# Performance work log

Hardware: AMD Instinct MI355X
Metric: run time of the kernel (lower is better)

The kernel has to match this reference:

```python
import jax, jax.numpy as jnp
from jax import lax
import numpy as np

HD = 256  # hidden_dim

def _conv(x, w, b=None, pad=1, groups=1):
    y = lax.conv_general_dilated(x, w, (1, 1), [(pad, pad), (pad, pad)],
                                 feature_group_count=groups,
                                 dimension_numbers=('NCHW', 'OIHW', 'NCHW'))
    return y if b is None else y + b[None, :, None, None]

def _maxpool2(x):
    return lax.reduce_window(x, -jnp.inf, lax.max, (1, 1, 2, 2), (1, 1, 2, 2), 'VALID')

def _up2(x):
    return jnp.repeat(jnp.repeat(x, 2, axis=2), 2, axis=3)

def setup_inputs() -> dict:
    key = jax.random.key(0)
    ks = jax.random.split(key, 17)
    w = lambda k, s: jax.random.normal(k, s, jnp.float32) * 0.05
    return {
        'x': jax.random.normal(ks[0], (8, 16, 3, 84, 84), jnp.float32),
        'enc_w1': w(ks[1], (64, 3, 3, 3)),    'enc_b1': w(ks[2], (64,)),
        'enc_w2': w(ks[3], (128, 64, 3, 3)),  'enc_b2': w(ks[4], (128,)),
        'enc_w3': w(ks[5], (256, 128, 3, 3)), 'enc_b3': w(ks[6], (256,)),
        'dw_w': w(ks[7], (512, 1, 3, 3)),
        'pw_w': w(ks[8], (1024, 512, 1, 1)),  'pw_b': w(ks[9], (1024,)),
        'dec_w1': w(ks[10], (128, 256, 3, 3)), 'dec_b1': w(ks[11], (128,)),
        'dec_w2': w(ks[12], (64, 128, 3, 3)),  'dec_b2': w(ks[13], (64,)),
        'dec_w3': w(ks[14], (1, 64, 1, 1)),    'dec_b3': w(ks[15], (1,)),
    }

def reference(x, enc_w1, enc_b1, enc_w2, enc_b2, enc_w3, enc_b3,
              dw_w, pw_w, pw_b, dec_w1, dec_b1, dec_w2, dec_b2, dec_w3, dec_b3):
    B, T, C, H, W = x.shape
    xf = x.reshape(B * T, C, H, W)
    # encoder: conv-relu-pool, conv-relu-pool, conv-relu
    f = _maxpool2(jax.nn.relu(_conv(xf, enc_w1, enc_b1)))
    f = _maxpool2(jax.nn.relu(_conv(f, enc_w2, enc_b2)))
    f = jax.nn.relu(_conv(f, enc_w3, enc_b3))           # [B*T, 256, 21, 21]
    Hf, Wf = f.shape[2], f.shape[3]
    feats = f.reshape(B, T, HD, Hf, Wf).transpose(1, 0, 2, 3, 4)  # [T,B,256,Hf,Wf]

    h0 = jnp.zeros((B, HD, Hf, Wf), x.dtype)
    c0 = jnp.zeros((B, HD, Hf, Wf), x.dtype)

    def step(carry, ft):
        h, c = carry
        comb = jnp.concatenate([ft, h], axis=1)          # [B, 512, Hf, Wf]
        g = _conv(comb, dw_w, None, pad=1, groups=comb.shape[1])  # depthwise
        g = _conv(g, pw_w, pw_b, pad=0)                  # pointwise -> 4*HD gates
        i, fg, o, gg = jnp.split(g, 4, axis=1)
        c2 = jax.nn.sigmoid(fg) * c + jax.nn.sigmoid(i) * jnp.tanh(gg)
        h2 = jax.nn.sigmoid(o) * jnp.tanh(c2)
        return (h2, c2), h2

    (h, c), hs = lax.scan(step, (h0, c0), feats)
    hs = hs.transpose(1, 0, 2, 3, 4).reshape(B * T, HD, Hf, Wf)

    # decoder: up2-conv-relu, up2-conv-relu, conv1x1
    d = jax.nn.relu(_conv(_up2(hs), dec_w1, dec_b1))     # [B*T, 128, 42, 42]
    d = jax.nn.relu(_conv(_up2(d), dec_w2, dec_b2))      # [B*T, 64, 84, 84]
    out = _conv(d, dec_w3, dec_b3, pad=0)                # [B*T, 1, 84, 84]
    out = out.reshape(B, T, 1, 84, 84)
    return out, h, c
```

## Files before the change

### kernel.cpp

```cpp
#include <hip/hip_runtime.h>
#include <hip/hip_bf16.h>

typedef __hip_bfloat16 bf16;
typedef __attribute__((ext_vector_type(8))) short bf16x8;
typedef __attribute__((ext_vector_type(4))) float f32x4;
#define DEV static __device__ __forceinline__

DEV float b2f(bf16 v) { return __bfloat162float(v); }
DEV bf16  f2b(float v) { return __float2bfloat16(v); }
DEV unsigned short f2u(float v) { bf16 t = f2b(v); return *(unsigned short*)&t; }
DEV float u2f(unsigned short u) { bf16 t = *(bf16*)&u; return __bfloat162float(t); }
DEV float sigf(float x) { return 1.0f / (1.0f + __expf(-x)); }
DEV float tanhfast(float x) { return 2.0f / (1.0f + __expf(-2.0f * x)) - 1.0f; }


__global__ void k_detect(const unsigned short* __restrict__ xb, int nscan, int* flag)
{
    __shared__ int cnt_s[256];
    int tid = threadIdx.x;
    int c = 0;
    for (int i = tid; i < nscan; i += 256) {
        unsigned int e = (xb[i] >> 7) & 0xFF;
        c += (e >= 0xC0);
    }
// ... 7 lines not shown
}

struct CanonSrc { const void* s[15]; };

__global__ __launch_bounds__(256) void k_canon_all(
    CanonSrc cs, char* __restrict__ wsb, int total, const int* __restrict__ flag)
{
    static const __device__ int off_d[16] = {0, 1728, 1792, 75520, 75648, 370560,
        370816, 375424, 899712, 900736, 1195648, 1195776, 1269504, 1269568,
        1269632, 1269633};
    static const __device__ long woff_d[15] = {0, 3456, 3584, 151040, 151296,
        741120, 741632, 750848, 1799424, 1801472, 2391296, 2391552, 2539008,
        2539136, 2539264};
    int i = blockIdx.x * 256 + threadIdx.x;
    if (i >= total) return;
    int t = 0;
    while (t < 14 && i >= off_d[t + 1]) ++t;
    int j = i - off_d[t];
    bf16* dst = (bf16*)(wsb + woff_d[t]);
    if (*flag) dst[j] = f2b(((const float*)cs.s[t])[j]);
    else       dst[j] = ((const bf16*)cs.s[t])[j];
}

__global__ __launch_bounds__(256) void k_combine1(
    const bf16* __restrict__ w, bf16* __restrict__ wc1)
{
    int idx = blockIdx.x * 256 + threadIdx.x;
    if (idx >= 524288) return;
    int ci = idx & 255, tap = (idx >> 8) & 3;
    int oc = (idx >> 10) & 127, par = idx >> 17;
    int a = tap >> 1, b = tap & 1;
    int py = par >> 1, px = par & 1;
    const bf16* wb = w + (oc * 256 + ci) * 9;
    float v = 0.f;
    #pragma unroll
    for (int ky = 0; ky < 3; ++ky) {
        bool rok = (py == 0) ? (a == 0 ? (ky == 0) : (ky >= 1))
                             : (a == 0 ? (ky <= 1) : (ky == 2));
        if (!rok) continue;
        #pragma unroll
        for (int kx = 0; kx < 3; ++kx) {
            bool cok = (px == 0) ? (b == 0 ? (kx == 0) : (kx >= 1))
                                 : (b == 0 ? (kx <= 1) : (kx == 2));
            if (cok) v += b2f(wb[ky * 3 + kx]);
        }
    }
    wc1[idx] = f2b(v);
}

__global__ __launch_bounds__(256) void k_combine2(
    const bf16* __restrict__ w, bf16* __restrict__ wc2)
{
    int idx = blockIdx.x * 256 + threadIdx.x;
    if (idx >= 131072) return;
    int ci = idx & 127, tap = (idx >> 7) & 3;
    int oc = (idx >> 9) & 63, par = idx >> 15;
    int a = tap >> 1, b = tap & 1;
    int py = par >> 1, px = par & 1;
    const bf16* wb = w + (oc * 128 + ci) * 9;
    float v = 0.f;
    #pragma unroll
    for (int ky = 0; ky < 3; ++ky) {
        bool rok = (py == 0) ? (a == 0 ? (ky == 0) : (ky >= 1))
                             : (a == 0 ? (ky <= 1) : (ky == 2));
        if (!rok) continue;
        #pragma unroll
        for (int kx = 0; kx < 3; ++kx) {
            bool cok = (px == 0) ? (b == 0 ? (kx == 0) : (kx >= 1))
                                 : (b == 0 ? (kx <= 1) : (kx == 2));
            if (cok) v += b2f(wb[ky * 3 + kx]);
        }
    }
    wc2[idx] = f2b(v);
}

__global__ __launch_bounds__(256) void k_prep_pw(
    const bf16* __restrict__ pww, bf16* __restrict__ wcp)
{
    int idx = blockIdx.x * 256 + threadIdx.x;
    if (idx >= 524288) return;
    int k = idx & 511, m = idx >> 9;
    int ch = m >> 2, gate = m & 3;
    wcp[idx] = pww[(gate * 256 + ch) * 512 + k];
}

__global__ __launch_bounds__(256) void k_prep_w3(
    const bf16* __restrict__ w, bf16* __restrict__ wc3)
{
    int idx = blockIdx.x * 256 + threadIdx.x;
    if (idx >= 294912) return;
    int oc = idx / 1152, rem = idx % 1152;
    int tap = rem >> 7, ci = rem & 127;
    wc3[idx] = w[(oc * 128 + ci) * 9 + tap];
}

__global__ __launch_bounds__(256) void k_prep_w2(
    const bf16* __restrict__ w, bf16* __restrict__ wc2e)
{
    int idx = blockIdx.x * 256 + threadIdx.x;
    if (idx >= 73728) return;
    int oc = idx / 576, rem = idx % 576;
    int tap = rem >> 6, ci = rem & 63;
    wc2e[idx] = w[(oc * 64 + ci) * 9 + tap];
}

__global__ __launch_bounds__(256) void k_prep_w1(
    const bf16* __restrict__ w, bf16* __restrict__ wc1e)
{
    int idx = blockIdx.x * 256 + threadIdx.x;
    if (idx >= 2048) return;
    int oc = idx >> 5, k = idx & 31;
    bf16 v = f2b(0.f);
    if (k < 27) v = w[oc * 27 + k];
    wc1e[idx] = v;
}

__global__ __launch_bounds__(256) void k_prep_dwt(
    const bf16* __restrict__ w, bf16* __restrict__ dwt)
{
    int idx = blockIdx.x * 256 + threadIdx.x;
    if (idx >= 4608) return;
    int tap = idx >> 9, ch = idx & 511;
    dwt[idx] = w[ch * 9 + tap];
}

__global__ __launch_bounds__(256) void k_conv1_mfma(
    const void* __restrict__ xv, const bf16* __restrict__ wc1e,
    const bf16* __restrict__ bias, bf16* __restrict__ p1c, int fbase,
    const int* __restrict__ flag)
{
    __shared__ __align__(16) short W_s[64 * 40];
    __shared__ __align__(16) short H_s[3 * 6 * 88];
    const int nt = blockIdx.x, z = blockIdx.z;
    const int n = fbase + z;
    const int tid = threadIdx.x;
    const int wave = tid >> 6, lane = tid & 63;
    const int quad = lane >> 4, nl = lane & 15;
    const int nn = wave * 16 + nl;
    const int p0 = nt * 63, y0 = p0 / 42;
    const int np = p0 + ((nn < 63) ? nn : 62);
    const int y = np / 42, xq = np % 42;
    const int isf32 = *flag;
    for (int u = tid; u < 256; u += 256) {
        int m = u >> 2, k8 = (u & 3) * 8;
        *(uint4*)&W_s[m * 40 + k8] = *(const uint4*)&wc1e[m * 32 + k8];
    }
// ... 40 lines not shown
    }
    if (nn < 63) {
        #pragma unroll
        for (int f = 0; f < 4; ++f) {
            ushort4 o;
            unsigned short* op = (unsigned short*)&o;
            #pragma unroll
            for (int reg = 0; reg < 4; ++reg) {
                const int oc = f * 16 + quad * 4 + reg;
                float m = fmaxf(fmaxf(acc[0][f][reg], acc[1][f][reg]),
                                fmaxf(acc[2][f][reg], acc[3][f][reg]));
                op[reg] = f2u(fmaxf(m + b2f(bias[oc]), 0.f));
            }
            *(ushort4*)&p1c[((long)z * 1764 + np) * 64 + f * 16 + quad * 4] = o;
        }
    }
}

__global__ __launch_bounds__(256) void k_conv2_mfma(
    const bf16* __restrict__ p1c, const bf16* __restrict__ wc2e,
    const bf16* __restrict__ bias, bf16* __restrict__ p2c)
{
    __shared__ __align__(16) short H_s[352 * 72];
    __shared__ __align__(16) short W_s[128 * 40];
    const int nt = blockIdx.x, z = blockIdx.z;
    const int tid = threadIdx.x;
    const int wave = tid >> 6, lane = tid & 63;
    const int quad = lane >> 4, nl = lane & 15;
    const int nn = wave * 16 + nl;
    const int np = (nn < 63) ? nn : 62;
    const int iyl = np / 21, ix = np % 21;
    const int r0 = nt * 3;
    for (int u = tid; u < 2816; u += 256) {
        int rc = u >> 3, c8 = u & 7;
        int gy = 2 * r0 - 1 + rc / 44, gx = (rc % 44) - 1;
        uint4 v = {0, 0, 0, 0};
        if (gy >= 0 && gy < 42 && gx >= 0 && gx < 42)
            v = *(const uint4*)&p1c[((long)z * 1764 + gy * 42 + gx) * 64 + c8 * 8];
        *(uint4*)&H_s[rc * 72 + c8 * 8] = v;
    }
    f32x4 acc[4][8];
    #pragma unroll
    for (int p = 0; p < 4; ++p)
        #pragma unroll
        for (int f = 0; f < 8; ++f) acc[p][f] = (f32x4){0.f, 0.f, 0.f, 0.f};
    for (int tap = 0; tap < 9; ++tap) {
        const int dy = tap / 3, dx = tap % 3;
        for (int cc = 0; cc < 2; ++cc) {
            __syncthreads();
            for (int u = tid; u < 512; u += 256) {
                int m = u >> 2, k8 = (u & 3) * 8;
                *(uint4*)&W_s[m * 40 + k8] =
                    *(const uint4*)&wc2e[m * 576 + tap * 64 + cc * 32 + k8];
            }
            __syncthreads();
            bf16x8 af[8];
            #pragma unroll
            for (int f = 0; f < 8; ++f)
                af[f] = *(const bf16x8*)&W_s[(f * 16 + nl) * 40 + quad * 8];
            #pragma unroll
            for (int par = 0; par < 4; ++par) {
                const int pa = par >> 1, pb = par & 1;
                const int hy = 2 * iyl + pa + dy;
                const int hx = 2 * ix + pb + dx;
                const bf16x8 bv =
                    *(const bf16x8*)&H_s[(hy * 44 + hx) * 72 + cc * 32 + quad * 8];
                #pragma unroll
                for (int f = 0; f < 8; ++f)
                    acc[par][f] = __builtin_amdgcn_mfma_f32_16x16x32_bf16(
                        af[f], bv, acc[par][f], 0, 0, 0);
            }
        }
    }
    if (nn < 63) {
        #pragma unroll
        for (int f = 0; f < 8; ++f) {
            ushort4 o;
            unsigned short* op = (unsigned short*)&o;
            #pragma unroll
            for (int reg = 0; reg < 4; ++reg) {
                const int oc = f * 16 + quad * 4 + reg;
                float m = fmaxf(fmaxf(acc[0][f][reg], acc[1][f][reg]),
                                fmaxf(acc[2][f][reg], acc[3][f][reg]));
                op[reg] = f2u(fmaxf(m + b2f(bias[oc]), 0.f));
            }
            *(ushort4*)&p2c[((long)z * 441 + (r0 + iyl) * 21 + ix) * 128 +
                            f * 16 + quad * 4] = o;
        }
    }
}

__global__ __launch_bounds__(256) void k_conv3_mfma(
    const bf16* __restrict__ p2c, const bf16* __restrict__ wc3,
    const bf16* __restrict__ bias, bf16* __restrict__ feats, int fbase)
{
    __shared__ __align__(16) short H_s[115 * 136];
    __shared__ __align__(16) short W_s[128 * 40];
    const int nt = blockIdx.x, oq = blockIdx.y, z = blockIdx.z;
    const int n = fbase + z;
    const int slot = (n & 15) * 8 + (n >> 4);
    const int tid = threadIdx.x;
    const int wave = tid >> 6, lane = tid & 63;
    const int quad = lane >> 4, nl = lane & 15;
    const int nn = wave * 16 + nl;
    const int np = (nn < 63) ? nn : 62;
    const int iyl = np / 21, ox = np % 21;
    const int r0 = nt * 3;
    for (int u = tid; u < 1840; u += 256) {
        int rc = u >> 4, c8 = u & 15;
        int gy = r0 + rc / 23 - 1, gx = (rc % 23) - 1;
        uint4 v = {0, 0, 0, 0};
        if (gy >= 0 && gy < 21 && gx >= 0 && gx < 21)
            v = *(const uint4*)&p2c[((long)z * 441 + gy * 21 + gx) * 128 + c8 * 8];
        *(uint4*)&H_s[rc * 136 + c8 * 8] = v;
    }
    f32x4 acc[8];
    #pragma unroll
    for (int f = 0; f < 8; ++f) acc[f] = (f32x4){0.f, 0.f, 0.f, 0.f};
    const int hb = iyl * 23 + ox;
    for (int tap = 0; tap < 9; ++tap) {
        const int dy = tap / 3, dx = tap % 3;
        const int hofs = (hb + dy * 23 + dx) * 136;
        for (int cc = 0; cc < 4; ++cc) {
            __syncthreads();
            for (int u = tid; u < 512; u += 256) {
                int m = u >> 2, k8 = (u & 3) * 8;
                *(uint4*)&W_s[m * 40 + k8] =
                    *(const uint4*)&wc3[(oq * 128 + m) * 1152 + tap * 128 + cc * 32 + k8];
            }
            __syncthreads();
            const bf16x8 bv = *(const bf16x8*)&H_s[hofs + cc * 32 + quad * 8];
            #pragma unroll
            for (int f = 0; f < 8; ++f) {
                bf16x8 af = *(const bf16x8*)&W_s[(f * 16 + nl) * 40 + quad * 8];
                acc[f] = __builtin_amdgcn_mfma_f32_16x16x32_bf16(af, bv, acc[f], 0, 0, 0);
            }
        }
    }
    if (nn < 63) {
        const int oy = r0 + iyl;
        #pragma unroll
        for (int f = 0; f < 8; ++f) {
            ushort4 o;
            unsigned short* op = (unsigned short*)&o;
            #pragma unroll
            for (int reg = 0; reg < 4; ++reg) {
                const int oc = oq * 128 + f * 16 + quad * 4 + reg;
                op[reg] = f2u(fmaxf(acc[f][reg] + b2f(bias[oc]), 0.f));
            }
            *(ushort4*)&feats[((long)slot * 441 + oy * 21 + ox) * 256 +
                              oq * 128 + f * 16 + quad * 4] = o;
        }
    }
}

__global__ __launch_bounds__(256) void k_dw_vec(
    const bf16* __restrict__ feats, const float* __restrict__ h,
    const bf16* __restrict__ dwt, bf16* __restrict__ dwout, int t)
{
    int idx = blockIdx.x * 256 + threadIdx.x;
// ... 29 lines not shown
                const float4 x1 = *(const float4*)&hb_[(ny * 21 + nx) * 256 + ch - 252];
                const float xf[8] = {x0.x, x0.y, x0.z, x0.w, x1.x, x1.y, x1.z, x1.w};
                #pragma unroll
                for (int j = 0; j < 8; ++j)
                    a8[j] += u2f(((unsigned short*)&wv)[j]) * xf[j];
            }
        }
    }
    ushort4 o0, o1;
    #pragma unroll
    for (int j = 0; j < 4; ++j) {
        ((unsigned short*)&o0)[j] = f2u(a8[j]);
        ((unsigned short*)&o1)[j] = f2u(a8[4 + j]);
    }
    *(ushort4*)&dwout[((long)b * 441 + p) * 512 + ch] = o0;
    *(ushort4*)&dwout[((long)b * 441 + p) * 512 + ch + 4] = o1;
}

__global__ __launch_bounds__(256) void k_pw_mfma(
    const bf16* __restrict__ dwout, const bf16* __restrict__ wcp,
    const bf16* __restrict__ pwb, float* __restrict__ h, float* __restrict__ c,
    bf16* __restrict__ hst)
{
    __shared__ __align__(16) short W_s[128 * 72];
    __shared__ __align__(16) short X_s[64 * 72];
    __shared__ bf16 pb_s[1024];
    const int nt = blockIdx.x, mq = blockIdx.y, b = blockIdx.z;
    const int tid = threadIdx.x;
    const int wave = tid >> 6, lane = tid & 63;
    const int quad = lane >> 4, nl = lane & 15;
    const int nn = wave * 16 + nl;
    for (int i = tid; i < 1024; i += 256) pb_s[i] = pwb[i];
    f32x4 acc[8];
    #pragma unroll
    for (int f = 0; f < 8; ++f) acc[f] = (f32x4){0.f, 0.f, 0.f, 0.f};
    for (int cc = 0; cc < 8; ++cc) {
        __syncthreads();
        for (int u = tid; u < 1024; u += 256) {
            int m = u >> 3, k8 = (u & 7) * 8;
            *(uint4*)&W_s[m * 72 + k8] =
                *(const uint4*)&wcp[(mq * 128 + m) * 512 + cc * 64 + k8];
        }
        for (int u = tid; u < 512; u += 256) {
            int p = u >> 3, k8 = (u & 7) * 8;
            int gp = nt * 63 + p;
            uint4 v = {0, 0, 0, 0};
            if (p < 63)
                v = *(const uint4*)&dwout[((long)b * 441 + gp) * 512 + cc * 64 + k8];
            *(uint4*)&X_s[p * 72 + k8] = v;
        }
        __syncthreads();
        #pragma unroll
        for (int s = 0; s < 2; ++s) {
            const bf16x8 bv = *(const bf16x8*)&X_s[nn * 72 + s * 32 + quad * 8];
            #pragma unroll
            for (int f = 0; f < 8; ++f) {
                bf16x8 af = *(const bf16x8*)&W_s[(f * 16 + nl) * 72 + s * 32 + quad * 8];
                acc[f] = __builtin_amdgcn_mfma_f32_16x16x32_bf16(af, bv, acc[f], 0, 0, 0);
            }
        }
    }
    if (nn < 63) {
        const int p = nt * 63 + nn;
        #pragma unroll
        for (int f = 0; f < 8; ++f) {
            const int ch = mq * 32 + f * 4 + quad;
            float ig = sigf(acc[f][0] + b2f(pb_s[ch]));
            float fg = sigf(acc[f][1] + b2f(pb_s[256 + ch]));
            float og = sigf(acc[f][2] + b2f(pb_s[512 + ch]));
            float gg = tanhfast(acc[f][3] + b2f(pb_s[768 + ch]));
            const int ci2 = (b * 441 + p) * 256 + ch;
            float c2 = fg * c[ci2] + ig * gg;
            float h2 = og * tanhfast(c2);
            c[ci2] = c2; h[ci2] = h2;
            hst[(long)b * 112896 + p * 256 + ch] = f2b(h2);
        }
    }
}

__global__ __launch_bounds__(256) void k_dec1_mfma(
    const bf16* __restrict__ feats, const bf16* __restrict__ hs0,
    const bf16* __restrict__ wc1, const bf16* __restrict__ bias,
    bf16* __restrict__ d1c, int c0f)
{
    __shared__ __align__(16) short H_s[184 * 72];
    __shared__ __align__(16) short W_s[128 * 72];
    const int nt = blockIdx.x, par = blockIdx.y, z = blockIdx.z;
    const int py = par >> 1, px = par & 1;
    const int n = c0f + z, bb = n >> 4, tt = n & 15;
    const short* hsf = (const short*)((tt == 0) ? (hs0 + (long)bb * 112896)
                        : (feats + (long)((tt - 1) * 8 + bb) * 112896));
    const int tid = threadIdx.x;
    const int wave = tid >> 6, lane = tid & 63;
    const int quad = lane >> 4, nl = lane & 15;
    int maxs = 440 - nt * 126; if (maxs > 125) maxs = 125;
    int hb[2], pv[2]; bool val[2];
    #pragma unroll
    for (int pg = 0; pg < 2; ++pg) {
        int slot = (wave * 2 + pg) * 16 + nl;
        val[pg] = (slot <= maxs);
        int sl = val[pg] ? slot : maxs;
        int p = nt * 126 + sl;
        pv[pg] = p;
        int y = p / 21, x = p % 21;
        hb[pg] = (y - nt * 6 + py) * 23 + (x + px);
    }
    f32x4 acc[2][8];
    #pragma unroll
    for (int pg = 0; pg < 2; ++pg)
        #pragma unroll
        for (int f = 0; f < 8; ++f) acc[pg][f] = (f32x4){0.f, 0.f, 0.f, 0.f};
    for (int cc = 0; cc < 4; ++cc) {
        __syncthreads();
        for (int u = tid; u < 1472; u += 256) {
            int rc = u >> 3, c8 = (u & 7) * 8;
            int gy = nt * 6 - 1 + rc / 23, gx = (rc % 23) - 1;
            uint4 v = {0, 0, 0, 0};
            if (gy >= 0 && gy < 21 && gx >= 0 && gx < 21)
                v = *(const uint4*)&hsf[(gy * 21 + gx) * 256 + cc * 64 + c8];
            *(uint4*)&H_s[rc * 72 + c8] = v;
        }
        for (int tap = 0; tap < 4; ++tap) {
            __syncthreads();
            for (int u = tid; u < 1024; u += 256) {
                int m = u >> 3, k8 = (u & 7) * 8;
                *(uint4*)&W_s[m * 72 + k8] =
                    *(const uint4*)&wc1[((par * 128 + m) << 10) + tap * 256 + cc * 64 + k8];
            }
            __syncthreads();
            const int a = tap >> 1, b = tap & 1;
            #pragma unroll
            for (int s = 0; s < 2; ++s) {
                bf16x8 bv0 = *(const bf16x8*)&H_s[(hb[0] + a * 23 + b) * 72 + s * 32 + quad * 8];
                bf16x8 bv1 = *(const bf16x8*)&H_s[(hb[1] + a * 23 + b) * 72 + s * 32 + quad * 8];
                #pragma unroll
                for (int f = 0; f < 8; ++f) {
                    bf16x8 af = *(const bf16x8*)&W_s[(f * 16 + nl) * 72 + s * 32 + quad * 8];
                    acc[0][f] = __builtin_amdgcn_mfma_f32_16x16x32_bf16(af, bv0, acc[0][f], 0, 0, 0);
                    acc[1][f] = __builtin_amdgcn_mfma_f32_16x16x32_bf16(af, bv1, acc[1][f], 0, 0, 0);
                }
            }
        }
    }
    #pragma unroll
    for (int pg = 0; pg < 2; ++pg) {
        if (!val[pg]) continue;
        const int p = pv[pg];
        const int oy = 2 * (p / 21) + py, ox = 2 * (p % 21) + px;
        #pragma unroll
        for (int f = 0; f < 8; ++f) {
            ushort4 o;
            unsigned short* op = (unsigned short*)&o;
            #pragma unroll
            for (int reg = 0; reg < 4; ++reg) {
                const int oc = f * 16 + quad * 4 + reg;
                op[reg] = f2u(fmaxf(acc[pg][f][reg] + b2f(bias[oc]), 0.f));
            }
            *(ushort4*)&d1c[((long)z * 1764 + oy * 42 + ox) * 128 +
                            f * 16 + quad * 4] = o;
        }
    }
}

__global__ __launch_bounds__(256) void k_dec2f_mfma(
    const bf16* __restrict__ d1c, const bf16* __restrict__ wc2,
    const bf16* __restrict__ bias, const bf16* __restrict__ w3,
    const bf16* __restrict__ b3, void* __restrict__ out, int c0f,
    const int* __restrict__ flag)
{
    __shared__ __align__(16) short H_s[220 * 72];
    __shared__ __align__(16) short W_s[64 * 72];
    const int nt = blockIdx.x, par = blockIdx.y, z = blockIdx.z;
    const int py = par >> 1, px = par & 1;
    const int tid = threadIdx.x;
    const int wave = tid >> 6, lane = tid & 63;
    const int quad = lane >> 4, nl = lane & 15;
    int hb[2], pv[2]; bool val[2];
    #pragma unroll
    for (int pg = 0; pg < 2; ++pg) {
        int slot = (wave * 2 + pg) * 16 + nl;
        val[pg] = (slot < 126);
        int sl = val[pg] ? slot : 125;
        int p = nt * 126 + sl;
        pv[pg] = p;
        int y = p / 42, x = p % 42;
        hb[pg] = (y - nt * 3 + py) * 44 + (x + px);
    }
    f32x4 acc[2][4];
    #pragma unroll
    for (int pg = 0; pg < 2; ++pg)
        #pragma unroll
        for (int f = 0; f < 4; ++f) acc[pg][f] = (f32x4){0.f, 0.f, 0.f, 0.f};
    for (int cc = 0; cc < 2; ++cc) {
        __syncthreads();
        for (int u = tid; u < 1760; u += 256) {
            int rc = u >> 3, c8 = (u & 7) * 8;
            int gy = nt * 3 - 1 + rc / 44, gx = (rc % 44) - 1;
            uint4 v = {0, 0, 0, 0};
            if (gy >= 0 && gy < 42 && gx >= 0 && gx < 42)
                v = *(const uint4*)&d1c[((long)z * 1764 + gy * 42 + gx) * 128 + cc * 64 + c8];
            *(uint4*)&H_s[rc * 72 + c8] = v;
        }
        for (int tap = 0; tap < 4; ++tap) {
            __syncthreads();
            for (int u = tid; u < 512; u += 256) {
                int m = u >> 3, k8 = (u & 7) * 8;
                *(uint4*)&W_s[m * 72 + k8] =
                    *(const uint4*)&wc2[((par * 64 + m) << 9) + tap * 128 + cc * 64 + k8];
            }
            __syncthreads();
            const int a = tap >> 1, b = tap & 1;
            #pragma unroll
            for (int s = 0; s < 2; ++s) {
                bf16x8 bv0 = *(const bf16x8*)&H_s[(hb[0] + a * 44 + b) * 72 + s * 32 + quad * 8];
                bf16x8 bv1 = *(const bf16x8*)&H_s[(hb[1] + a * 44 + b) * 72 + s * 32 + quad * 8];
                #pragma unroll
                for (int f = 0; f < 4; ++f) {
                    bf16x8 af = *(const bf16x8*)&W_s[(f * 16 + nl) * 72 + s * 32 + quad * 8];
                    acc[0][f] = __builtin_amdgcn_mfma_f32_16x16x32_bf16(af, bv0, acc[0][f], 0, 0, 0);
                    acc[1][f] = __builtin_amdgcn_mfma_f32_16x16x32_bf16(af, bv1, acc[1][f], 0, 0, 0);
                }
            }
        }
    }
    #pragma unroll
    for (int pg = 0; pg < 2; ++pg) {
        float part = 0.f;
        #pragma unroll
        for (int f = 0; f < 4; ++f)
            #pragma unroll
            for (int reg = 0; reg < 4; ++reg) {
                const int oc = f * 16 + quad * 4 + reg;
                part += b2f(w3[oc]) * fmaxf(acc[pg][f][reg] + b2f(bias[oc]), 0.f);
            }
        part += __shfl_xor(part, 16);
        part += __shfl_xor(part, 32);
        if (quad == 0 && val[pg]) {
            const int p = pv[pg];
            const int oy = 2 * (p / 42) + py, ox = 2 * (p % 42) + px;
            const float v = part + b2f(b3[0]);
            const long oi = (long)(c0f + z) * 7056 + oy * 84 + ox;
            if (*flag) ((float*)out)[oi] = v;
            else       ((bf16*)out)[oi]  = f2b(v);
        }
    }
// ... 21 lines not shown
extern "C" void kernel_launch(void* const* d_in, const int* in_sizes, int n_in,
                              void* d_out, int out_size, void* d_ws, size_t ws_size,
                              hipStream_t stream)
{
    char* wsb = (char*)d_ws;
    static const long woff[15] = {0, 3456, 3584, 151040, 151296, 741120, 741632,
                                  750848, 1799424, 1801472, 2391296, 2391552,
                                  2539008, 2539136, 2539264};
    const long FLAG_OFF = 2539280;
    const long WC1_OFF = 2539296;
    const long WC2_OFF = 3587872;
    const long WCP_OFF = 3850016;
    const long WC3_OFF = 4898592;
    const long WC2E_OFF = 5488416;
    const long WC1E_OFF = 5635872;
    const long DWT_OFF  = 5639968;
    const long CE = 5649184;
    int* flag = (int*)(wsb + FLAG_OFF);

    k_detect<<<1, 256, 0, stream>>>((const unsigned short*)d_in[0], 8192, flag);
    CanonSrc cs;
    for (int i = 0; i < 15; ++i) cs.s[i] = d_in[i + 1];
    k_canon_all<<<(1269633 + 255) / 256, 256, 0, stream>>>(cs, wsb, 1269633, flag);

    const void* x = d_in[0];
    bf16 *enc_b1 = (bf16*)(wsb + woff[1]),
         *enc_b2 = (bf16*)(wsb + woff[3]),
         *enc_w1 = (bf16*)(wsb + woff[0]),
         *enc_w2 = (bf16*)(wsb + woff[2]),
         *enc_w3 = (bf16*)(wsb + woff[4]), *enc_b3 = (bf16*)(wsb + woff[5]),
         *dw_w   = (bf16*)(wsb + woff[6]), *pw_w   = (bf16*)(wsb + woff[7]),
         *pw_b   = (bf16*)(wsb + woff[8]), *dec_w1 = (bf16*)(wsb + woff[9]),
         *dec_b1 = (bf16*)(wsb + woff[10]), *dec_w2 = (bf16*)(wsb + woff[11]),
         *dec_b2 = (bf16*)(wsb + woff[12]), *dec_w3 = (bf16*)(wsb + woff[13]),
         *dec_b3 = (bf16*)(wsb + woff[14]);
    bf16* wc1  = (bf16*)(wsb + WC1_OFF);
    bf16* wc2  = (bf16*)(wsb + WC2_OFF);
    bf16* wcp  = (bf16*)(wsb + WCP_OFF);
    bf16* wc3  = (bf16*)(wsb + WC3_OFF);
    bf16* wc2e = (bf16*)(wsb + WC2E_OFF);
    bf16* wc1e = (bf16*)(wsb + WC1E_OFF);
    bf16* dwt  = (bf16*)(wsb + DWT_OFF);

    k_combine1<<<2048, 256, 0, stream>>>(dec_w1, wc1);
    k_combine2<<<512, 256, 0, stream>>>(dec_w2, wc2);
    k_prep_pw<<<2048, 256, 0, stream>>>(pw_w, wcp);
    k_prep_w3<<<1152, 256, 0, stream>>>(enc_w3, wc3);
    k_prep_w2<<<288, 256, 0, stream>>>(enc_w2, wc2e);
    k_prep_w1<<<8, 256, 0, stream>>>(enc_w1, wc1e);
    k_prep_dwt<<<18, 256, 0, stream>>>(dw_w, dwt);

    bf16*  feats = (bf16*)(wsb + CE);
    bf16*  hs0   = (bf16*)(wsb + CE + 28901376);
    float* hbuf  = (float*)(wsb + CE + 30707712);
    float* cbuf  = (float*)(wsb + CE + 34320384);
    bf16*  d1c   = (bf16*)(wsb + CE + 37933056);
    bf16*  p1c   = (bf16*)(wsb + CE + 37933056);
    bf16*  p2c   = (bf16*)(wsb + CE + 28901376);
    bf16*  dwout = (bf16*)(wsb + CE + 52383744);

    for (int f0 = 0; f0 < 128; f0 += 64) {
        k_conv1_mfma<<<dim3(28, 1, 64), 256, 0, stream>>>(x, wc1e, enc_b1, p1c, f0, flag);
        k_conv2_mfma<<<dim3(7, 1, 64), 256, 0, stream>>>(p1c, wc2e, enc_b2, p2c);
        k_conv3_mfma<<<dim3(7, 2, 64), 256, 0, stream>>>(p2c, wc3, enc_b3, feats, f0);
    }
    hipMemsetAsync(hbuf, 0, 2 * 3612672, stream);
    for (int t = 0; t < 16; ++t) {
        bf16* hst = (t == 0) ? hs0 : (feats + (long)(t - 1) * 8 * 112896);
        k_dw_vec<<<882, 256, 0, stream>>>(feats, hbuf, dwt, dwout, t);
        k_pw_mfma<<<dim3(7, 8, 8), 256, 0, stream>>>(dwout, wcp, pw_b, hbuf, cbuf, hst);
    }
    k_out_hc<<<3528, 256, 0, stream>>>(hbuf, cbuf, d_out, flag);
    for (int c0f = 0; c0f < 128; c0f += 32) {
        k_dec1_mfma<<<dim3(4, 4, 32), 256, 0, stream>>>(feats, hs0, wc1, dec_b1, d1c, c0f);
// ... 5 lines not shown
```

Before: 1.420 ms.

## Double-buffer weight tiles in MFMA conv/GEMM kernels and merge weight prep kernels

The encoder conv2/conv3, pointwise gate GEMM and decoder conv kernels now keep two LDS weight buffers. The next K-chunk is loaded into registers while MFMAs run on the current chunk, which halves the __syncthreads per iteration. In the decoder convs the input halo tile is reloaded only when the channel chunk changes. The seven weight-preparation kernels are merged into one launch with hardcoded offsets. LDS use per block goes up, which may lower occupancy, and the extra prefetch registers add register pressure.

After: 1.249 ms. 12.1% less time.

```diff
diff --git a/kernel.cpp b/kernel.cpp
--- a/kernel.cpp
+++ b/kernel.cpp
@@ -53,106 +53,91 @@
     else       dst[j] = ((const bf16*)cs.s[t])[j];
 }
 
-__global__ __launch_bounds__(256) void k_combine1(
-    const bf16* __restrict__ w, bf16* __restrict__ wc1)
-{
-    int idx = blockIdx.x * 256 + threadIdx.x;
-    if (idx >= 524288) return;
-    int ci = idx & 255, tap = (idx >> 8) & 3;
-    int oc = (idx >> 10) & 127, par = idx >> 17;
-    int a = tap >> 1, b = tap & 1;
-    int py = par >> 1, px = par & 1;
-    const bf16* wb = w + (oc * 256 + ci) * 9;
-    float v = 0.f;
-    #pragma unroll
-    for (int ky = 0; ky < 3; ++ky) {
-        bool rok = (py == 0) ? (a == 0 ? (ky == 0) : (ky >= 1))
-                             : (a == 0 ? (ky <= 1) : (ky == 2));
-        if (!rok) continue;
-        #pragma unroll
-        for (int kx = 0; kx < 3; ++kx) {
-            bool cok = (px == 0) ? (b == 0 ? (kx == 0) : (kx >= 1))
-                                 : (b == 0 ? (kx <= 1) : (kx == 2));
-            if (cok) v += b2f(wb[ky * 3 + kx]);
-        }
-    }
-    wc1[idx] = f2b(v);
-}
-
-__global__ __launch_bounds__(256) void k_combine2(
-    const bf16* __restrict__ w, bf16* __restrict__ wc2)
-{
-    int idx = blockIdx.x * 256 + threadIdx.x;
-    if (idx >= 131072) return;
-    int ci = idx & 127, tap = (idx >> 7) & 3;
-    int oc = (idx >> 9) & 63, par = idx >> 15;
-    int a = tap >> 1, b = tap & 1;
-    int py = par >> 1, px = par & 1;
-    const bf16* wb = w + (oc * 128 + ci) * 9;
-    float v = 0.f;
-    #pragma unroll
-    for (int ky = 0; ky < 3; ++ky) {
-        bool rok = (py == 0) ? (a == 0 ? (ky == 0) : (ky >= 1))
-                             : (a == 0 ? (ky <= 1) : (ky == 2));
-        if (!rok) continue;
-        #pragma unroll
-        for (int kx = 0; kx < 3; ++kx) {
-            bool cok = (px == 0) ? (b == 0 ? (kx == 0) : (kx >= 1))
-                                 : (b == 0 ? (kx <= 1) : (kx == 2));
-            if (cok) v += b2f(wb[ky * 3 + kx]);
-        }
-    }
-    wc2[idx] = f2b(v);
-}
-
-__global__ __launch_bounds__(256) void k_prep_pw(
-    const bf16* __restrict__ pww, bf16* __restrict__ wcp)
-{
-    int idx = blockIdx.x * 256 + threadIdx.x;
-    if (idx >= 524288) return;
-    int k = idx & 511, m = idx >> 9;
-    int ch = m >> 2, gate = m & 3;
-    wcp[idx] = pww[(gate * 256 + ch) * 512 + k];
-}
-
-__global__ __launch_bounds__(256) void k_prep_w3(
-    const bf16* __restrict__ w, bf16* __restrict__ wc3)
-{
-    int idx = blockIdx.x * 256 + threadIdx.x;
-    if (idx >= 294912) return;
-    int oc = idx / 1152, rem = idx % 1152;
-    int tap = rem >> 7, ci = rem & 127;
-    wc3[idx] = w[(oc * 128 + ci) * 9 + tap];
-}
-
-__global__ __launch_bounds__(256) void k_prep_w2(
-    const bf16* __restrict__ w, bf16* __restrict__ wc2e)
-{
-    int idx = blockIdx.x * 256 + threadIdx.x;
-    if (idx >= 73728) return;
-    int oc = idx / 576, rem = idx % 576;
-    int tap = rem >> 6, ci = rem & 63;
-    wc2e[idx] = w[(oc * 64 + ci) * 9 + tap];
-}
-
-__global__ __launch_bounds__(256) void k_prep_w1(
-    const bf16* __restrict__ w, bf16* __restrict__ wc1e)
-{
-    int idx = blockIdx.x * 256 + threadIdx.x;
-    if (idx >= 2048) return;
-    int oc = idx >> 5, k = idx & 31;
-    bf16 v = f2b(0.f);
-    if (k < 27) v = w[oc * 27 + k];
-    wc1e[idx] = v;
-}
-
-__global__ __launch_bounds__(256) void k_prep_dwt(
-    const bf16* __restrict__ w, bf16* __restrict__ dwt)
-{
-    int idx = blockIdx.x * 256 + threadIdx.x;
-    if (idx >= 4608) return;
-    int tap = idx >> 9, ch = idx & 511;
-    dwt[idx] = w[ch * 9 + tap];
+__global__ __launch_bounds__(256) void k_prep_all(char* __restrict__ wsb)
+{
+    long gid = (long)blockIdx.x * 256 + threadIdx.x;
+    if (gid < 524288) {
+        int idx = (int)gid;
+        const bf16* w = (const bf16*)(wsb + 1801472);
+        bf16* wc1 = (bf16*)(wsb + 2539296);
+        int ci = idx & 255, tap = (idx >> 8) & 3;
+        int oc = (idx >> 10) & 127, par = idx >> 17;
+        int a = tap >> 1, b = tap & 1;
+        int py = par >> 1, px = par & 1;
+        const bf16* wb = w + (oc * 256 + ci) * 9;
+        float v = 0.f;
+        #pragma unroll
+        for (int ky = 0; ky < 3; ++ky) {
+            bool rok = (py == 0) ? (a == 0 ? (ky == 0) : (ky >= 1))
+                                 : (a == 0 ? (ky <= 1) : (ky == 2));
+            if (!rok) continue;
+            #pragma unroll
+            for (int kx = 0; kx < 3; ++kx) {
+                bool cok = (px == 0) ? (b == 0 ? (kx == 0) : (kx >= 1))
+                                     : (b == 0 ? (kx <= 1) : (kx == 2));
+                if (cok) v += b2f(wb[ky * 3 + kx]);
+            }
+        }
+        wc1[idx] = f2b(v);
+    } else if (gid < 655360) {
+        int idx = (int)(gid - 524288);
+        const bf16* w = (const bf16*)(wsb + 2391552);
+        bf16* wc2 = (bf16*)(wsb + 3587872);
+        int ci = idx & 127, tap = (idx >> 7) & 3;
+        int oc = (idx >> 9) & 63, par = idx >> 15;
+        int a = tap >> 1, b = tap & 1;
+        int py = par >> 1, px = par & 1;
+        const bf16* wb = w + (oc * 128 + ci) * 9;
+        float v = 0.f;
+        #pragma unroll
+        for (int ky = 0; ky < 3; ++ky) {
+            bool rok = (py == 0) ? (a == 0 ? (ky == 0) : (ky >= 1))
+                                 : (a == 0 ? (ky <= 1) : (ky == 2));
+            if (!rok) continue;
+            #pragma unroll
+            for (int kx = 0; kx < 3; ++kx) {
+                bool cok = (px == 0) ? (b == 0 ? (kx == 0) : (kx >= 1))
+                                     : (b == 0 ? (kx <= 1) : (kx == 2));
+                if (cok) v += b2f(wb[ky * 3 + kx]);
+            }
+        }
+        wc2[idx] = f2b(v);
+    } else if (gid < 1179648) {
+        int idx = (int)(gid - 655360);
+        const bf16* pww = (const bf16*)(wsb + 750848);
+        bf16* wcp = (bf16*)(wsb + 3850016);
+        int k = idx & 511, m = idx >> 9;
+        int ch = m >> 2, gate = m & 3;
+        wcp[idx] = pww[(gate * 256 + ch) * 512 + k];
+    } else if (gid < 1474560) {
+        int idx = (int)(gid - 1179648);
+        const bf16* w = (const bf16*)(wsb + 151296);
+        bf16* wc3 = (bf16*)(wsb + 4898592);
+        int oc = idx / 1152, rem = idx % 1152;
+        int tap = rem >> 7, ci = rem & 127;
+        wc3[idx] = w[(oc * 128 + ci) * 9 + tap];
+    } else if (gid < 1548288) {
+        int idx = (int)(gid - 1474560);
+        const bf16* w = (const bf16*)(wsb + 3584);
+        bf16* wc2e = (bf16*)(wsb + 5488416);
+        int oc = idx / 576, rem = idx % 576;
+        int tap = rem >> 6, ci = rem & 63;
+        wc2e[idx] = w[(oc * 64 + ci) * 9 + tap];
+    } else if (gid < 1550336) {
+        int idx = (int)(gid - 1548288);
+        const bf16* w = (const bf16*)(wsb + 0);
+        bf16* wc1e = (bf16*)(wsb + 5635872);
+        int oc = idx >> 5, k = idx & 31;
+        bf16 v = f2b(0.f);
+        if (k < 27) v = w[oc * 27 + k];
+        wc1e[idx] = v;
+    } else if (gid < 1554944) {
+        int idx = (int)(gid - 1550336);
+        const bf16* w = (const bf16*)(wsb + 741632);
+        bf16* dwt = (bf16*)(wsb + 5639968);
+        int tap = idx >> 9, ch = idx & 511;
+        dwt[idx] = w[ch * 9 + tap];
+    }
 }
 
 __global__ __launch_bounds__(256) void k_conv1_mfma(
@@ -239,7 +224,7 @@
     const bf16* __restrict__ bias, bf16* __restrict__ p2c)
 {
     __shared__ __align__(16) short H_s[352 * 72];
-    __shared__ __align__(16) short W_s[128 * 40];
+    __shared__ __align__(16) short W_s[2][128 * 40];
     const int nt = blockIdx.x, z = blockIdx.z;
     const int tid = threadIdx.x;
     const int wave = tid >> 6, lane = tid & 63;
@@ -256,38 +241,50 @@
             v = *(const uint4*)&p1c[((long)z * 1764 + gy * 42 + gx) * 64 + c8 * 8];
         *(uint4*)&H_s[rc * 72 + c8 * 8] = v;
     }
+    const int m0 = tid >> 2, k80 = (tid & 3) * 8;
+    const int m1 = (tid + 256) >> 2, k81 = ((tid + 256) & 3) * 8;
+    *(uint4*)&W_s[0][m0 * 40 + k80] = *(const uint4*)&wc2e[m0 * 576 + k80];
+    *(uint4*)&W_s[0][m1 * 40 + k81] = *(const uint4*)&wc2e[m1 * 576 + k81];
+    __syncthreads();
     f32x4 acc[4][8];
     #pragma unroll
     for (int p = 0; p < 4; ++p)
         #pragma unroll
         for (int f = 0; f < 8; ++f) acc[p][f] = (f32x4){0.f, 0.f, 0.f, 0.f};
-    for (int tap = 0; tap < 9; ++tap) {
+    for (int it = 0; it < 18; ++it) {
+        const int tap = it >> 1, cc = it & 1;
+        const bool ld = (it + 1 < 18);
+        uint4 wr0, wr1;
+        if (ld) {
+            const int ntap = (it + 1) >> 1, ncc = (it + 1) & 1;
+            const bf16* src = wc2e + ntap * 64 + ncc * 32;
+            wr0 = *(const uint4*)&src[m0 * 576 + k80];
+            wr1 = *(const uint4*)&src[m1 * 576 + k81];
+        }
         const int dy = tap / 3, dx = tap % 3;
-        for (int cc = 0; cc < 2; ++cc) {
-            __syncthreads();
-            for (int u = tid; u < 512; u += 256) {
-                int m = u >> 2, k8 = (u & 3) * 8;
-                *(uint4*)&W_s[m * 40 + k8] =
-                    *(const uint4*)&wc2e[m * 576 + tap * 64 + cc * 32 + k8];
-            }
-            __syncthreads();
-            bf16x8 af[8];
+        const short* Wc = W_s[it & 1];
+        bf16x8 af[8];
+        #pragma unroll
+        for (int f = 0; f < 8; ++f)
+            af[f] = *(const bf16x8*)&Wc[(f * 16 + nl) * 40 + quad * 8];
+        #pragma unroll
+        for (int par = 0; par < 4; ++par) {
+            const int pa = par >> 1, pb = par & 1;
+            const int hy = 2 * iyl + pa + dy;
+            const int hx = 2 * ix + pb + dx;
+            const bf16x8 bv =
+                *(const bf16x8*)&H_s[(hy * 44 + hx) * 72 + cc * 32 + quad * 8];
             #pragma unroll
             for (int f = 0; f < 8; ++f)
-                af[f] = *(const bf16x8*)&W_s[(f * 16 + nl) * 40 + quad * 8];
-            #pragma unroll
-            for (int par = 0; par < 4; ++par) {
-                const int pa = par >> 1, pb = par & 1;
-                const int hy = 2 * iyl + pa + dy;
-                const int hx = 2 * ix + pb + dx;
-                const bf16x8 bv =
-                    *(const bf16x8*)&H_s[(hy * 44 + hx) * 72 + cc * 32 + quad * 8];
-                #pragma unroll
-                for (int f = 0; f < 8; ++f)
-                    acc[par][f] = __builtin_amdgcn_mfma_f32_16x16x32_bf16(
-                        af[f], bv, acc[par][f], 0, 0, 0);
-            }
-        }
+                acc[par][f] = __builtin_amdgcn_mfma_f32_16x16x32_bf16(
+                    af[f], bv, acc[par][f], 0, 0, 0);
+        }
+        if (ld) {
+            short* Wn = W_s[(it + 1) & 1];
+            *(uint4*)&Wn[m0 * 40 + k80] = wr0;
+            *(uint4*)&Wn[m1 * 40 + k81] = wr1;
+        }
+        __syncthreads();
     }
     if (nn < 63) {
         #pragma unroll
@@ -312,7 +309,7 @@
     const bf16* __restrict__ bias, bf16* __restrict__ feats, int fbase)
 {
     __shared__ __align__(16) short H_s[115 * 136];
-    __shared__ __align__(16) short W_s[128 * 40];
+    __shared__ __align__(16) short W_s[2][128 * 40];
     const int nt = blockIdx.x, oq = blockIdx.y, z = blockIdx.z;
     const int n = fbase + z;
     const int slot = (n & 15) * 8 + (n >> 4);
@@ -331,28 +328,41 @@
             v = *(const uint4*)&p2c[((long)z * 441 + gy * 21 + gx) * 128 + c8 * 8];
         *(uint4*)&H_s[rc * 136 + c8 * 8] = v;
     }
+    const bf16* wbase = wc3 + (long)(oq * 128) * 1152;
+    const int m0 = tid >> 2, k80 = (tid & 3) * 8;
+    const int m1 = (tid + 256) >> 2, k81 = ((tid + 256) & 3) * 8;
+    *(uint4*)&W_s[0][m0 * 40 + k80] = *(const uint4*)&wbase[m0 * 1152 + k80];
+    *(uint4*)&W_s[0][m1 * 40 + k81] = *(const uint4*)&wbase[m1 * 1152 + k81];
+    __syncthreads();
     f32x4 acc[8];
     #pragma unroll
     for (int f = 0; f < 8; ++f) acc[f] = (f32x4){0.f, 0.f, 0.f, 0.f};
     const int hb = iyl * 23 + ox;
-    for (int tap = 0; tap < 9; ++tap) {
+    for (int it = 0; it < 36; ++it) {
+        const int tap = it >> 2, cc = it & 3;
+        const bool ld = (it + 1 < 36);
+        uint4 wr0, wr1;
+        if (ld) {
+            const int ntap = (it + 1) >> 2, ncc = (it + 1) & 3;
+            const bf16* src = wbase + ntap * 128 + ncc * 32;
+            wr0 = *(const uint4*)&src[m0 * 1152 + k80];
+            wr1 = *(const uint4*)&src[m1 * 1152 + k81];
+        }
         const int dy = tap / 3, dx = tap % 3;
         const int hofs = (hb + dy * 23 + dx) * 136;
-        for (int cc = 0; cc < 4; ++cc) {
-            __syncthreads();
-            for (int u = tid; u < 512; u += 256) {
-                int m = u >> 2, k8 = (u & 3) * 8;
-                *(uint4*)&W_s[m * 40 + k8] =
-                    *(const uint4*)&wc3[(oq * 128 + m) * 1152 + tap * 128 + cc * 32 + k8];
-            }
-            __syncthreads();
-            const bf16x8 bv = *(const bf16x8*)&H_s[hofs + cc * 32 + quad * 8];
-            #pragma unroll
-            for (int f = 0; f < 8; ++f) {
-                bf16x8 af = *(const bf16x8*)&W_s[(f * 16 + nl) * 40 + quad * 8];
-                acc[f] = __builtin_amdgcn_mfma_f32_16x16x32_bf16(af, bv, acc[f], 0, 0, 0);
-            }
-        }
+        const bf16x8 bv = *(const bf16x8*)&H_s[hofs + cc * 32 + quad * 8];
+        const short* Wc = W_s[it & 1];
+        #pragma unroll
+        for (int f = 0; f < 8; ++f) {
+            bf16x8 af = *(const bf16x8*)&Wc[(f * 16 + nl) * 40 + quad * 8];
+            acc[f] = __builtin_amdgcn_mfma_f32_16x16x32_bf16(af, bv, acc[f], 0, 0, 0);
+        }
+        if (ld) {
+            short* Wn = W_s[(it + 1) & 1];
+            *(uint4*)&Wn[m0 * 40 + k80] = wr0;
+            *(uint4*)&Wn[m1 * 40 + k81] = wr1;
+        }
+        __syncthreads();
     }
     if (nn < 63) {
         const int oy = r0 + iyl;
@@ -428,8 +438,8 @@
     const bf16* __restrict__ pwb, float* __restrict__ h, float* __restrict__ c,
     bf16* __restrict__ hst)
 {
-    __shared__ __align__(16) short W_s[128 * 72];
-    __shared__ __align__(16) short X_s[64 * 72];
+    __shared__ __align__(16) short W_s[2][128 * 72];
+    __shared__ __align__(16) short X_s[2][64 * 72];
     __shared__ bf16 pb_s[1024];
     const int nt = blockIdx.x, mq = blockIdx.y, b = blockIdx.z;
     const int tid = threadIdx.x;
@@ -437,34 +447,61 @@
     const int quad = lane >> 4, nl = lane & 15;
     const int nn = wave * 16 + nl;
     for (int i = tid; i < 1024; i += 256) pb_s[i] = pwb[i];
+    const bf16* wb = wcp + (long)(mq * 128) * 512;
+    const bf16* xb = dwout + ((long)b * 441 + nt * 63) * 512;
+    int wm[4], wk[4];
+    #pragma unroll
+    for (int i = 0; i < 4; ++i) { int u = tid + 256 * i; wm[i] = u >> 3; wk[i] = (u & 7) * 8; }
+    int xp[2], xk[2];
+    #pragma unroll
+    for (int i = 0; i < 2; ++i) { int u = tid + 256 * i; xp[i] = u >> 3; xk[i] = (u & 7) * 8; }
+    #pragma unroll
+    for (int i = 0; i < 4; ++i)
+        *(uint4*)&W_s[0][wm[i] * 72 + wk[i]] = *(const uint4*)&wb[wm[i] * 512 + wk[i]];
+    #pragma unroll
+    for (int i = 0; i < 2; ++i) {
+        uint4 v = {0, 0, 0, 0};
+        if (xp[i] < 63) v = *(const uint4*)&xb[xp[i] * 512 + xk[i]];
+        *(uint4*)&X_s[0][xp[i] * 72 + xk[i]] = v;
+    }
+    __syncthreads();
     f32x4 acc[8];
     #pragma unroll
     for (int f = 0; f < 8; ++f) acc[f] = (f32x4){0.f, 0.f, 0.f, 0.f};
     for (int cc = 0; cc < 8; ++cc) {
+        const bool ld = (cc + 1 < 8);
+        uint4 wr[4], xr[2];
+        if (ld) {
+            #pragma unroll
+            for (int i = 0; i < 4; ++i)
+                wr[i] = *(const uint4*)&wb[wm[i] * 512 + (cc + 1) * 64 + wk[i]];
+            #pragma unroll
+            for (int i = 0; i < 2; ++i) {
+                uint4 v = {0, 0, 0, 0};
+                if (xp[i] < 63) v = *(const uint4*)&xb[xp[i] * 512 + (cc + 1) * 64 + xk[i]];
+                xr[i] = v;
+            }
+        }
+        const short* Wc = W_s[cc & 1];
+        const short* Xc = X_s[cc & 1];
+        #pragma unroll
+        for (int s = 0; s < 2; ++s) {
+            const bf16x8 bv = *(const bf16x8*)&Xc[nn * 72 + s * 32 + quad * 8];
+            #pragma unroll
+            for (int f = 0; f < 8; ++f) {
+                bf16x8 af = *(const bf16x8*)&Wc[(f * 16 + nl) * 72 + s * 32 + quad * 8];
+                acc[f] = __builtin_amdgcn_mfma_f32_16x16x32_bf16(af, bv, acc[f], 0, 0, 0);
+            }
+        }
+        if (ld) {
+            short* Wn = W_s[(cc + 1) & 1];
+            short* Xn = X_s[(cc + 1) & 1];
+            #pragma unroll
+            for (int i = 0; i < 4; ++i) *(uint4*)&Wn[wm[i] * 72 + wk[i]] = wr[i];
+            #pragma unroll
+            for (int i = 0; i < 2; ++i) *(uint4*)&Xn[xp[i] * 72 + xk[i]] = xr[i];
+        }
         __syncthreads();
-        for (int u = tid; u < 1024; u += 256) {
-            int m = u >> 3, k8 = (u & 7) * 8;
-            *(uint4*)&W_s[m * 72 + k8] =
-                *(const uint4*)&wcp[(mq * 128 + m) * 512 + cc * 64 + k8];
-        }
-        for (int u = tid; u < 512; u += 256) {
-            int p = u >> 3, k8 = (u & 7) * 8;
-            int gp = nt * 63 + p;
-            uint4 v = {0, 0, 0, 0};
-            if (p < 63)
-                v = *(const uint4*)&dwout[((long)b * 441 + gp) * 512 + cc * 64 + k8];
-            *(uint4*)&X_s[p * 72 + k8] = v;
-        }
-        __syncthreads();
-        #pragma unroll
-        for (int s = 0; s < 2; ++s) {
-            const bf16x8 bv = *(const bf16x8*)&X_s[nn * 72 + s * 32 + quad * 8];
-            #pragma unroll
-            for (int f = 0; f < 8; ++f) {
-                bf16x8 af = *(const bf16x8*)&W_s[(f * 16 + nl) * 72 + s * 32 + quad * 8];
-                acc[f] = __builtin_amdgcn_mfma_f32_16x16x32_bf16(af, bv, acc[f], 0, 0, 0);
-            }
-        }
     }
     if (nn < 63) {
         const int p = nt * 63 + nn;
@@ -490,7 +527,7 @@
     bf16* __restrict__ d1c, int c0f)
 {
     __shared__ __align__(16) short H_s[184 * 72];
-    __shared__ __align__(16) short W_s[128 * 72];
+    __shared__ __align__(16) short W_s[2][128 * 72];
     const int nt = blockIdx.x, par = blockIdx.y, z = blockIdx.z;
     const int py = par >> 1, px = par & 1;
     const int n = c0f + z, bb = n >> 4, tt = n & 15;
@@ -511,41 +548,67 @@
         int y = p / 21, x = p % 21;
         hb[pg] = (y - nt * 6 + py) * 23 + (x + px);
     }
+    const bf16* wbase = wc1 + ((long)(par * 128) << 10);
+    int wm[4], wk[4];
+    #pragma unroll
+    for (int i = 0; i < 4; ++i) { int u = tid + 256 * i; wm[i] = u >> 3; wk[i] = (u & 7) * 8; }
+    for (int u = tid; u < 1472; u += 256) {
+        int rc = u >> 3, c8 = (u & 7) * 8;
+        int gy = nt * 6 - 1 + rc / 23, gx = (rc % 23) - 1;
+        uint4 v = {0, 0, 0, 0};
+        if (gy >= 0 && gy < 21 && gx >= 0 && gx < 21)
+            v = *(const uint4*)&hsf[(gy * 21 + gx) * 256 + c8];
+        *(uint4*)&H_s[rc * 72 + c8] = v;
+    }
+    #pragma unroll
+    for (int i = 0; i < 4; ++i)
+        *(uint4*)&W_s[0][wm[i] * 72 + wk[i]] = *(const uint4*)&wbase[wm[i] * 1024 + wk[i]];
+    __syncthreads();
     f32x4 acc[2][8];
     #pragma unroll
     for (int pg = 0; pg < 2; ++pg)
         #pragma unroll
         for (int f = 0; f < 8; ++f) acc[pg][f] = (f32x4){0.f, 0.f, 0.f, 0.f};
-    for (int cc = 0; cc < 4; ++cc) {
+    for (int it = 0; it < 16; ++it) {
+        const int cc = it >> 2, tap = it & 3;
+        const bool ld = (it + 1 < 16);
+        uint4 wr[4];
+        if (ld) {
+            const int ncc = (it + 1) >> 2, ntap = (it + 1) & 3;
+            const bf16* src = wbase + ntap * 256 + ncc * 64;
+            #pragma unroll
+            for (int i = 0; i < 4; ++i)
+                wr[i] = *(const uint4*)&src[wm[i] * 1024 + wk[i]];
+        }
+        const int a = tap >> 1, b = tap & 1;
+        const short* Wc = W_s[it & 1];
+        #pragma unroll
+        for (int s = 0; s < 2; ++s) {
+            bf16x8 bv0 = *(const bf16x8*)&H_s[(hb[0] + a * 23 + b) * 72 + s * 32 + quad * 8];
+            bf16x8 bv1 = *(const bf16x8*)&H_s[(hb[1] + a * 23 + b) * 72 + s * 32 + quad * 8];
+            #pragma unroll
+            for (int f = 0; f < 8; ++f) {
+                bf16x8 af = *(const bf16x8*)&Wc[(f * 16 + nl) * 72 + s * 32 + quad * 8];
+                acc[0][f] = __builtin_amdgcn_mfma_f32_16x16x32_bf16(af, bv0, acc[0][f], 0, 0, 0);
+                acc[1][f] = __builtin_amdgcn_mfma_f32_16x16x32_bf16(af, bv1, acc[1][f], 0, 0, 0);
+            }
+        }
+        if (ld) {
+            short* Wn = W_s[(it + 1) & 1];
+            #pragma unroll
+            for (int i = 0; i < 4; ++i) *(uint4*)&Wn[wm[i] * 72 + wk[i]] = wr[i];
+        }
         __syncthreads();
-        for (int u = tid; u < 1472; u += 256) {
-            int rc = u >> 3, c8 = (u & 7) * 8;
-            int gy = nt * 6 - 1 + rc / 23, gx = (rc % 23) - 1;
-            uint4 v = {0, 0, 0, 0};
-            if (gy >= 0 && gy < 21 && gx >= 0 && gx < 21)
-                v = *(const uint4*)&hsf[(gy * 21 + gx) * 256 + cc * 64 + c8];
-            *(uint4*)&H_s[rc * 72 + c8] = v;
-        }
-        for (int tap = 0; tap < 4; ++tap) {
+        if (tap == 3 && cc < 3) {
+            for (int u = tid; u < 1472; u += 256) {
+                int rc = u >> 3, c8 = (u & 7) * 8;
+                int gy = nt * 6 - 1 + rc / 23, gx = (rc % 23) - 1;
+                uint4 v = {0, 0, 0, 0};
+                if (gy >= 0 && gy < 21 && gx >= 0 && gx < 21)
+                    v = *(const uint4*)&hsf[(gy * 21 + gx) * 256 + (cc + 1) * 64 + c8];
+                *(uint4*)&H_s[rc * 72 + c8] = v;
+            }
             __syncthreads();
-            for (int u = tid; u < 1024; u += 256) {
-                int m = u >> 3, k8 = (u & 7) * 8;
-                *(uint4*)&W_s[m * 72 + k8] =
-                    *(const uint4*)&wc1[((par * 128 + m) << 10) + tap * 256 + cc * 64 + k8];
-            }
-            __syncthreads();
-            const int a = tap >> 1, b = tap & 1;
-            #pragma unroll
-            for (int s = 0; s < 2; ++s) {
-                bf16x8 bv0 = *(const bf16x8*)&H_s[(hb[0] + a * 23 + b) * 72 + s * 32 + quad * 8];
-                bf16x8 bv1 = *(const bf16x8*)&H_s[(hb[1] + a * 23 + b) * 72 + s * 32 + quad * 8];
-                #pragma unroll
-                for (int f = 0; f < 8; ++f) {
-                    bf16x8 af = *(const bf16x8*)&W_s[(f * 16 + nl) * 72 + s * 32 + quad * 8];
-                    acc[0][f] = __builtin_amdgcn_mfma_f32_16x16x32_bf16(af, bv0, acc[0][f], 0, 0, 0);
-                    acc[1][f] = __builtin_amdgcn_mfma_f32_16x16x32_bf16(af, bv1, acc[1][f], 0, 0, 0);
-                }
-            }
         }
     }
     #pragma unroll
@@ -575,7 +638,7 @@
     const int* __restrict__ flag)
 {
     __shared__ __align__(16) short H_s[220 * 72];
-    __shared__ __align__(16) short W_s[64 * 72];
+    __shared__ __align__(16) short W_s[2][64 * 72];
     const int nt = blockIdx.x, par = blockIdx.y, z = blockIdx.z;
     const int py = par >> 1, px = par & 1;
     const int tid = threadIdx.x;
@@ -592,41 +655,64 @@
         int y = p / 42, x = p % 42;
         hb[pg] = (y - nt * 3 + py) * 44 + (x + px);
     }
+    const bf16* wbase = wc2 + ((long)(par * 64) << 9);
+    const int wm0 = tid >> 3, wk0 = (tid & 7) * 8;
+    const int wm1 = (tid + 256) >> 3, wk1 = ((tid + 256) & 7) * 8;
+    for (int u = tid; u < 1760; u += 256) {
+        int rc = u >> 3, c8 = (u & 7) * 8;
+        int gy = nt * 3 - 1 + rc / 44, gx = (rc % 44) - 1;
+        uint4 v = {0, 0, 0, 0};
+        if (gy >= 0 && gy < 42 && gx >= 0 && gx < 42)
+            v = *(const uint4*)&d1c[((long)z * 1764 + gy * 42 + gx) * 128 + c8];
+        *(uint4*)&H_s[rc * 72 + c8] = v;
+    }
+    *(uint4*)&W_s[0][wm0 * 72 + wk0] = *(const uint4*)&wbase[wm0 * 512 + wk0];
+    *(uint4*)&W_s[0][wm1 * 72 + wk1] = *(const uint4*)&wbase[wm1 * 512 + wk1];
+    __syncthreads();
     f32x4 acc[2][4];
     #pragma unroll
     for (int pg = 0; pg < 2; ++pg)
         #pragma unroll
         for (int f = 0; f < 4; ++f) acc[pg][f] = (f32x4){0.f, 0.f, 0.f, 0.f};
-    for (int cc = 0; cc < 2; ++cc) {
+    for (int it = 0; it < 8; ++it) {
+        const int cc = it >> 2, tap = it & 3;
+        const bool ld = (it + 1 < 8);
+        uint4 wr0, wr1;
+        if (ld) {
+            const int ncc = (it + 1) >> 2, ntap = (it + 1) & 3;
+            const bf16* src = wbase + ntap * 128 + ncc * 64;
+            wr0 = *(const uint4*)&src[wm0 * 512 + wk0];
+            wr1 = *(const uint4*)&src[wm1 * 512 + wk1];
+        }
+        const int a = tap >> 1, b = tap & 1;
+        const short* Wc = W_s[it & 1];
+        #pragma unroll
+        for (int s = 0; s < 2; ++s) {
+            bf16x8 bv0 = *(const bf16x8*)&H_s[(hb[0] + a * 44 + b) * 72 + s * 32 + quad * 8];
+            bf16x8 bv1 = *(const bf16x8*)&H_s[(hb[1] + a * 44 + b) * 72 + s * 32 + quad * 8];
+            #pragma unroll
+            for (int f = 0; f < 4; ++f) {
+                bf16x8 af = *(const bf16x8*)&Wc[(f * 16 + nl) * 72 + s * 32 + quad * 8];
+                acc[0][f] = __builtin_amdgcn_mfma_f32_16x16x32_bf16(af, bv0, acc[0][f], 0, 0, 0);
+                acc[1][f] = __builtin_amdgcn_mfma_f32_16x16x32_bf16(af, bv1, acc[1][f], 0, 0, 0);
+            }
+        }
+        if (ld) {
+            short* Wn = W_s[(it + 1) & 1];
+            *(uint4*)&Wn[wm0 * 72 + wk0] = wr0;
+            *(uint4*)&Wn[wm1 * 72 + wk1] = wr1;
+        }
         __syncthreads();
-        for (int u = tid; u < 1760; u += 256) {
-            int rc = u >> 3, c8 = (u & 7) * 8;
-            int gy = nt * 3 - 1 + rc / 44, gx = (rc % 44) - 1;
-            uint4 v = {0, 0, 0, 0};
-            if (gy >= 0 && gy < 42 && gx >= 0 && gx < 42)
-                v = *(const uint4*)&d1c[((long)z * 1764 + gy * 42 + gx) * 128 + cc * 64 + c8];
-            *(uint4*)&H_s[rc * 72 + c8] = v;
-        }
-        for (int tap = 0; tap < 4; ++tap) {
+        if (tap == 3 && cc == 0) {
+            for (int u = tid; u < 1760; u += 256) {
+                int rc = u >> 3, c8 = (u & 7) * 8;
+                int gy = nt * 3 - 1 + rc / 44, gx = (rc % 44) - 1;
+                uint4 v = {0, 0, 0, 0};
+                if (gy >= 0 && gy < 42 && gx >= 0 && gx < 42)
+                    v = *(const uint4*)&d1c[((long)z * 1764 + gy * 42 + gx) * 128 + 64 + c8];
+                *(uint4*)&H_s[rc * 72 + c8] = v;
+            }
             __syncthreads();
-            for (int u = tid; u < 512; u += 256) {
-                int m = u >> 3, k8 = (u & 7) * 8;
-                *(uint4*)&W_s[m * 72 + k8] =
-                    *(const uint4*)&wc2[((par * 64 + m) << 9) + tap * 128 + cc * 64 + k8];
-            }
-            __syncthreads();
-            const int a = tap >> 1, b = tap & 1;
-            #pragma unroll
-            for (int s = 0; s < 2; ++s) {
-                bf16x8 bv0 = *(const bf16x8*)&H_s[(hb[0] + a * 44 + b) * 72 + s * 32 + quad * 8];
-                bf16x8 bv1 = *(const bf16x8*)&H_s[(hb[1] + a * 44 + b) * 72 + s * 32 + quad * 8];
-                #pragma unroll
-                for (int f = 0; f < 4; ++f) {
-                    bf16x8 af = *(const bf16x8*)&W_s[(f * 16 + nl) * 72 + s * 32 + quad * 8];
-                    acc[0][f] = __builtin_amdgcn_mfma_f32_16x16x32_bf16(af, bv0, acc[0][f], 0, 0, 0);
-                    acc[1][f] = __builtin_amdgcn_mfma_f32_16x16x32_bf16(af, bv1, acc[1][f], 0, 0, 0);
-                }
-            }
         }
     }
     #pragma unroll
@@ -694,16 +780,13 @@
     CanonSrc cs;
     for (int i = 0; i < 15; ++i) cs.s[i] = d_in[i + 1];
     k_canon_all<<<(1269633 + 255) / 256, 256, 0, stream>>>(cs, wsb, 1269633, flag);
+    k_prep_all<<<6074, 256, 0, stream>>>(wsb);
 
     const void* x = d_in[0];
     bf16 *enc_b1 = (bf16*)(wsb + woff[1]),
-         *enc_b2 = (bf16*)(wsb + woff[3]),
-         *enc_w1 = (bf16*)(wsb + woff[0]),
-         *enc_w2 = (bf16*)(wsb + woff[2]),
-         *enc_w3 = (bf16*)(wsb + woff[4]), *enc_b3 = (bf16*)(wsb + woff[5]),
-         *dw_w   = (bf16*)(wsb + woff[6]), *pw_w   = (bf16*)(wsb + woff[7]),
-         *pw_b   = (bf16*)(wsb + woff[8]), *dec_w1 = (bf16*)(wsb + woff[9]),
-         *dec_b1 = (bf16*)(wsb + woff[10]), *dec_w2 = (bf16*)(wsb + woff[11]),
+         *enc_b2 = (bf16*)(wsb + woff[3]), *enc_b3 = (bf16*)(wsb + woff[5]),
+         *pw_b   = (bf16*)(wsb + woff[8]),
+         *dec_b1 = (bf16*)(wsb + woff[10]),
          *dec_b2 = (bf16*)(wsb + woff[12]), *dec_w3 = (bf16*)(wsb + woff[13]),
          *dec_b3 = (bf16*)(wsb + woff[14]);
     bf16* wc1  = (bf16*)(wsb + WC1_OFF);
@@ -714,14 +797,6 @@
     bf16* wc1e = (bf16*)(wsb + WC1E_OFF);
     bf16* dwt  = (bf16*)(wsb + DWT_OFF);
 
-    k_combine1<<<2048, 256, 0, stream>>>(dec_w1, wc1);
-    k_combine2<<<512, 256, 0, stream>>>(dec_w2, wc2);
-    k_prep_pw<<<2048, 256, 0, stream>>>(pw_w, wcp);
-    k_prep_w3<<<1152, 256, 0, stream>>>(enc_w3, wc3);
-    k_prep_w2<<<288, 256, 0, stream>>>(enc_w2, wc2e);
-    k_prep_w1<<<8, 256, 0, stream>>>(enc_w1, wc1e);
-    k_prep_dwt<<<18, 256, 0, stream>>>(dw_w, dwt);
-
     bf16*  feats = (bf16*)(wsb + CE);
     bf16*  hs0   = (bf16*)(wsb + CE + 28901376);
     float* hbuf  = (float*)(wsb + CE + 30707712);
```
